# Optimization experiments

Measured on AMD Instinct MI355X. Metric: run time of the kernel, lower is better.

The kernel has to match this reference:

```python
import jax, jax.numpy as jnp
import numpy as np

B, N, D, H = 32, 64, 128, 256

def setup_inputs() -> dict:
    key = jax.random.key(0)
    ks = jax.random.split(key, 6)
    s = 0.02
    return {
        "objects": jax.random.normal(ks[0], (B, N, D), dtype=jnp.float32),
        "gW1": jax.random.normal(ks[1], (2 * D, H), dtype=jnp.float32) * s,
        "gb1": jnp.zeros((H,), dtype=jnp.float32),
        "gW2": jax.random.normal(ks[2], (H, H), dtype=jnp.float32) * s,
        "gb2": jnp.zeros((H,), dtype=jnp.float32),
        "gW3": jax.random.normal(ks[3], (H, H), dtype=jnp.float32) * s,
        "gb3": jnp.zeros((H,), dtype=jnp.float32),
        "fW1": jax.random.normal(ks[4], (H, H), dtype=jnp.float32) * s,
        "fb1": jnp.zeros((H,), dtype=jnp.float32),
        "fW2": jax.random.normal(ks[5], (H, H), dtype=jnp.float32) * s,
        "fb2": jnp.zeros((H,), dtype=jnp.float32),
    }

def reference(objects, gW1, gb1, gW2, gb2, gW3, gb3, fW1, fb1, fW2, fb2):
    b, n, d = objects.shape
    # Pairwise concat: pair[b,i,j] = [objects[b,i], objects[b,j]] -> (B,N,N,2D)
    left = jnp.broadcast_to(objects[:, :, None, :], (b, n, n, d))
    right = jnp.broadcast_to(objects[:, None, :, :], (b, n, n, d))
    pair = jnp.concatenate([left, right], axis=-1)
    # g_theta: 3-layer MLP with ReLU after first two layers
    h = jax.nn.relu(pair @ gW1 + gb1)
    h = jax.nn.relu(h @ gW2 + gb2)
    h = h @ gW3 + gb3                      # (B,N,N,H)
    # Sum over all pairs i != j
    mask = (1.0 - jnp.eye(n, dtype=h.dtype))  # (N,N)
    agg = jnp.einsum('bijh,ij->bh', h, mask)  # (B,H)
    # f_phi: Linear-ReLU-Linear
    out = jax.nn.relu(agg @ fW1 + fb1) @ fW2 + fb2
    return out
```

## Files before the change

### kernel.cpp

```cpp
#include <hip/hip_runtime.h>
#include <hip/hip_bf16.h>

typedef __attribute__((ext_vector_type(8))) _Float16 half8;
typedef __attribute__((ext_vector_type(4))) float f32x4;

union PrepShared {
    struct { float so[8 * 128]; float tt[64 * 65]; } a;
    struct { float sg[8 * 256]; float ps[4][8][256]; } m;
};

__global__ __launch_bounds__(256) void rn_prep(
    const float* __restrict__ obj, const float* __restrict__ gW1,
    const float* __restrict__ gb1, const float* __restrict__ gW2,
    const float* __restrict__ gW3, const float* __restrict__ gb3,
    const float* __restrict__ fW1, const float* __restrict__ fb1,
    _Float16* __restrict__ Lh, _Float16* __restrict__ Rh,
    _Float16* __restrict__ W2h, float* __restrict__ S,
    float* __restrict__ M, float* __restrict__ dvec)
{
    __shared__ PrepShared sh;
    const int blk = blockIdx.x, t = threadIdx.x;

    if (blk < 256) {
        float* so = sh.a.so;
        const int r0 = blk * 8;
        #pragma unroll
        for (int it = 0; it < 4; ++it) so[it * 256 + t] = obj[r0 * 128 + it * 256 + t];
        __syncthreads();
        float accL[8], accR[8];
        #pragma unroll
        for (int r = 0; r < 8; ++r) { accL[r] = 0.f; accR[r] = 0.f; }
        for (int k = 0; k < 128; ++k) {
            float wL = gW1[k * 256 + t];
            float wR = gW1[(128 + k) * 256 + t];
            #pragma unroll
            for (int r = 0; r < 8; ++r) {
                float o = so[r * 128 + k];
                accL[r] += o * wL;
                accR[r] += o * wR;
            }
        }
        float bb = gb1[t];
        #pragma unroll
        for (int r = 0; r < 8; ++r) {
            int row = r0 + r;
            Lh[row * 256 + t] = (_Float16)(accL[r] + bb);
            Rh[row * 256 + t] = (_Float16)accR[r];
        }
    } else if (blk < 272) {
        float* tt = sh.a.tt;
        const int tb = blk - 256;
        const int k0 = (tb >> 2) * 64, c0 = (tb & 3) * 64;
        for (int it = 0; it < 16; ++it) {
            int idx = it * 256 + t, rr = idx >> 6, cc = idx & 63;
            tt[rr * 65 + cc] = gW2[(k0 + rr) * 256 + c0 + cc];
        }
        __syncthreads();
        for (int it = 0; it < 16; ++it) {
            int idx = it * 256 + t, cr = idx >> 6, kk = idx & 63;
            W2h[(c0 + cr) * 256 + (k0 + kk)] = (_Float16)tt[kk * 65 + cr];
        }
    } else if (blk == 272) {
        for (int it = 0; it < 32; ++it) S[it * 256 + t] = 0.f;
        const int cg = t & 63, jq = t >> 6, c0 = cg * 4;
        f32x4 a = (f32x4){0.f, 0.f, 0.f, 0.f};
        #pragma unroll 8
        for (int jj = 0; jj < 64; ++jj) {
            int j = jq * 64 + jj;
            a += gb3[j] * (*(const f32x4*)&fW1[j * 256 + c0]);
        }
        *(f32x4*)&sh.m.ps[jq][0][c0] = a;
        __syncthreads();
        float s = sh.m.ps[0][0][t] + sh.m.ps[1][0][t] + sh.m.ps[2][0][t] + sh.m.ps[3][0][t];
        dvec[t] = 4032.0f * s + fb1[t];
    } else {
        float* sg = sh.m.sg;
        const int r0 = (blk - 273) * 8;
        const int cg = t & 63, jq = t >> 6, c0 = cg * 4;
        #pragma unroll
        for (int it = 0; it < 8; ++it) sg[it * 256 + t] = gW3[(r0 + it) * 256 + t];
        __syncthreads();
        f32x4 acc[8];
        #pragma unroll
        for (int r = 0; r < 8; ++r) acc[r] = (f32x4){0.f, 0.f, 0.f, 0.f};
        #pragma unroll 8
        for (int jj = 0; jj < 64; ++jj) {
            int j = jq * 64 + jj;
            f32x4 wv = *(const f32x4*)&fW1[j * 256 + c0];
            #pragma unroll
            for (int r = 0; r < 8; ++r) acc[r] += sg[r * 256 + j] * wv;
        }
        #pragma unroll
        for (int r = 0; r < 8; ++r) *(f32x4*)&sh.m.ps[jq][r][c0] = acc[r];
        __syncthreads();
        #pragma unroll
        for (int r = 0; r < 8; ++r)
            M[(r0 + r) * 256 + t] =
                sh.m.ps[0][r][t] + sh.m.ps[1][r][t] + sh.m.ps[2][r][t] + sh.m.ps[3][r][t];
    }
}

__global__ __launch_bounds__(512, 1) void rn_main(
    const _Float16* __restrict__ Lh, const _Float16* __restrict__ Rh,
    const _Float16* __restrict__ W2h, const float* __restrict__ gb2,
    float* __restrict__ S)
{
    const int blk = blockIdx.x;
    const int b = blk >> 3, ig = blk & 7;
    const int t = threadIdx.x, lane = t & 63, w = t >> 6;
    const int mg = w >> 2, ng = w & 3;
    const int lc = lane & 15, lg = lane >> 4;

    half8 bfr[4][8];
    #pragma unroll
    for (int n = 0; n < 4; ++n)
        #pragma unroll
        for (int ks = 0; ks < 8; ++ks)
            bfr[n][ks] = *(const half8*)(W2h + (ng * 64 + n * 16 + lc) * 256 + ks * 32 + lg * 8);

    half8 rh[2][8];
    #pragma unroll
    for (int m2 = 0; m2 < 2; ++m2) {
        int row = b * 64 + mg * 32 + m2 * 16 + lc;
        #pragma unroll
        for (int ks = 0; ks < 8; ++ks)
            rh[m2][ks] = *(const half8*)(Rh + row * 256 + ks * 32 + lg * 8);
    }

    float bias[4];
    #pragma unroll
    for (int n = 0; n < 4; ++n) bias[n] = gb2[ng * 64 + n * 16 + lc];

    const _Float16* lbase = Lh + (b * 64 + ig * 8) * 256;
    const half8 zero8 = {(_Float16)0.f, (_Float16)0.f, (_Float16)0.f, (_Float16)0.f,
                         (_Float16)0.f, (_Float16)0.f, (_Float16)0.f, (_Float16)0.f};
    const f32x4 zero4 = (f32x4){0.f, 0.f, 0.f, 0.f};
    float csum[4] = {0.f, 0.f, 0.f, 0.f};

    #pragma unroll 1
    for (int ii = 0; ii < 8; ++ii) {
        f32x4 acc[2][4];
        #pragma unroll
        for (int m2 = 0; m2 < 2; ++m2)
            #pragma unroll
            for (int n = 0; n < 4; ++n)
                acc[m2][n] = zero4;

        #pragma unroll
        for (int ks = 0; ks < 8; ++ks) {
            half8 lhv = *(const half8*)(lbase + ii * 256 + ks * 32 + lg * 8);
            #pragma unroll
            for (int m2 = 0; m2 < 2; ++m2) {
                half8 av = __builtin_elementwise_max(lhv + rh[m2][ks], zero8);
                #pragma unroll
                for (int n = 0; n < 4; ++n)
                    acc[m2][n] = __builtin_amdgcn_mfma_f32_16x16x32_f16(
                        av, bfr[n][ks], acc[m2][n], 0, 0, 0);
            }
        }

        const int iglob = ig * 8 + ii;
        #pragma unroll
        for (int n = 0; n < 4; ++n) {
            #pragma unroll
            for (int m2 = 0; m2 < 2; ++m2) {
                #pragma unroll
                for (int q = 0; q < 4; ++q) {
                    int row = mg * 32 + m2 * 16 + lg * 4 + q;
                    float v = fmaxf(acc[m2][n][q] + bias[n], 0.f);
                    csum[n] += (row == iglob) ? 0.f : v;
                }
            }
        }
    }

    #pragma unroll
    for (int n = 0; n < 4; ++n) {
        float cs = csum[n];
        cs += __shfl_xor(cs, 16);
        cs += __shfl_xor(cs, 32);
        if (lane < 16) atomicAdd(&S[b * 256 + ng * 64 + n * 16 + lc], cs);
    }
}

__global__ __launch_bounds__(1024) void rn_final(
    const float* __restrict__ S, const float* __restrict__ M,
    const float* __restrict__ dvec, const float* __restrict__ fW2,
    const float* __restrict__ fb2, float* __restrict__ out)
{
    __shared__ float vec[256];
    __shared__ float ps[16][260];
    const int b = blockIdx.x, t = threadIdx.x;
    const int cg = t & 63, kq = t >> 6;
    const int c0 = cg * 4;

    if (t < 256) vec[t] = S[b * 256 + t];
    __syncthreads();

    f32x4 w2r[16];
    {
        f32x4 s = (f32x4){0.f, 0.f, 0.f, 0.f};
        #pragma unroll
        for (int kk = 0; kk < 16; ++kk) {
            int k = kq * 16 + kk;
            s += (*(const f32x4*)&M[k * 256 + c0]) * vec[k];
        }
        *(f32x4*)&ps[kq][c0] = s;
        #pragma unroll
        for (int kk = 0; kk < 16; ++kk)
            w2r[kk] = *(const f32x4*)&fW2[(kq * 16 + kk) * 256 + c0];
    }
    __syncthreads();
    if (t < 256) {
        float a = 0.f;
        #pragma unroll
        for (int q = 0; q < 16; ++q) a += ps[q][t];
        vec[t] = fmaxf(a + dvec[t], 0.f);
    }
    __syncthreads();

    {
        f32x4 s = (f32x4){0.f, 0.f, 0.f, 0.f};
        #pragma unroll
        for (int kk = 0; kk < 16; ++kk)
            s += w2r[kk] * vec[kq * 16 + kk];
        *(f32x4*)&ps[kq][c0] = s;
    }
    __syncthreads();
    if (t < 256) {
        float a = 0.f;
        #pragma unroll
        for (int q = 0; q < 16; ++q) a += ps[q][t];
        out[b * 256 + t] = a + fb2[t];
    }
}

extern "C" void kernel_launch(void* const* d_in, const int* in_sizes, int n_in,
                              void* d_out, int out_size, void* d_ws, size_t ws_size,
                              hipStream_t stream)
{
    const float* obj = (const float*)d_in[0];
    const float* gW1 = (const float*)d_in[1];
    const float* gb1 = (const float*)d_in[2];
    const float* gW2 = (const float*)d_in[3];
    const float* gb2 = (const float*)d_in[4];
    const float* gW3 = (const float*)d_in[5];
    const float* gb3 = (const float*)d_in[6];
    const float* fW1 = (const float*)d_in[7];
    const float* fb1 = (const float*)d_in[8];
    const float* fW2 = (const float*)d_in[9];
    const float* fb2 = (const float*)d_in[10];
    float* out = (float*)d_out;

    char* ws = (char*)d_ws;
    _Float16* Lh  = (_Float16*)(ws);
    _Float16* Rh  = (_Float16*)(ws + (1u << 20));
    _Float16* W2h = (_Float16*)(ws + (2u << 20));
    float*    S   = (float*)(ws + (2u << 20) + (128u << 10));
    float*    M   = (float*)(ws + (2u << 20) + (160u << 10));
    float*    dv  = (float*)(ws + (2u << 20) + (416u << 10));

    rn_prep <<<305, 256, 0, stream>>>(obj, gW1, gb1, gW2, gW3, gb3, fW1, fb1,
                                      Lh, Rh, W2h, S, M, dv);
    rn_main <<<256, 512, 0, stream>>>(Lh, Rh, W2h, gb2, S);
    rn_final<<<32, 1024, 0, stream>>>(S, M, dv, fW2, fb2, out);
}
```

Baseline: 52.70 us.

## Stage swizzled R/L tiles in LDS and replace atomics with partial sums

The prep kernel now uses twice as many blocks with 4 rows each, and writes Rh in an XOR-swizzled layout. The main kernel cooperatively loads the batch's R rows and the block's L rows into shared memory and reads them back with the swizzle, avoiding bank conflicts. Per-block column sums are stored to a partial buffer instead of going through atomicAdd, so S no longer has to be zeroed. The final kernel reduces the 16 partials. Launch bounds now allow 2 blocks per CU, which may push the register budget of the main kernel.

```diff
diff --git a/kernel.cpp b/kernel.cpp
--- a/kernel.cpp
+++ b/kernel.cpp
@@ -5,7 +5,7 @@
 typedef __attribute__((ext_vector_type(4))) float f32x4;
 
 union PrepShared {
-    struct { float so[8 * 128]; float tt[64 * 65]; } a;
+    struct { float so[4 * 128]; float tt[64 * 65]; } a;
     struct { float sg[8 * 256]; float ps[4][8][256]; } m;
 };
 
@@ -14,27 +14,26 @@
     const float* __restrict__ gb1, const float* __restrict__ gW2,
     const float* __restrict__ gW3, const float* __restrict__ gb3,
     const float* __restrict__ fW1, const float* __restrict__ fb1,
-    _Float16* __restrict__ Lh, _Float16* __restrict__ Rh,
-    _Float16* __restrict__ W2h, float* __restrict__ S,
-    float* __restrict__ M, float* __restrict__ dvec)
+    _Float16* __restrict__ Lh, char* __restrict__ RhB,
+    _Float16* __restrict__ W2h, float* __restrict__ M, float* __restrict__ dvec)
 {
     __shared__ PrepShared sh;
     const int blk = blockIdx.x, t = threadIdx.x;
 
-    if (blk < 256) {
+    if (blk < 512) {
         float* so = sh.a.so;
-        const int r0 = blk * 8;
-        #pragma unroll
-        for (int it = 0; it < 4; ++it) so[it * 256 + t] = obj[r0 * 128 + it * 256 + t];
-        __syncthreads();
-        float accL[8], accR[8];
-        #pragma unroll
-        for (int r = 0; r < 8; ++r) { accL[r] = 0.f; accR[r] = 0.f; }
+        const int r0 = blk * 4;
+        #pragma unroll
+        for (int it = 0; it < 2; ++it) so[it * 256 + t] = obj[r0 * 128 + it * 256 + t];
+        __syncthreads();
+        float accL[4], accR[4];
+        #pragma unroll
+        for (int r = 0; r < 4; ++r) { accL[r] = 0.f; accR[r] = 0.f; }
         for (int k = 0; k < 128; ++k) {
             float wL = gW1[k * 256 + t];
             float wR = gW1[(128 + k) * 256 + t];
             #pragma unroll
-            for (int r = 0; r < 8; ++r) {
+            for (int r = 0; r < 4; ++r) {
                 float o = so[r * 128 + k];
                 accL[r] += o * wL;
                 accR[r] += o * wR;
@@ -42,14 +41,14 @@
         }
         float bb = gb1[t];
         #pragma unroll
-        for (int r = 0; r < 8; ++r) {
+        for (int r = 0; r < 4; ++r) {
             int row = r0 + r;
             Lh[row * 256 + t] = (_Float16)(accL[r] + bb);
-            Rh[row * 256 + t] = (_Float16)accR[r];
-        }
-    } else if (blk < 272) {
+            *(_Float16*)(RhB + row * 512 + ((2 * t) ^ ((row & 15) << 4))) = (_Float16)accR[r];
+        }
+    } else if (blk < 528) {
         float* tt = sh.a.tt;
-        const int tb = blk - 256;
+        const int tb = blk - 512;
         const int k0 = (tb >> 2) * 64, c0 = (tb & 3) * 64;
         for (int it = 0; it < 16; ++it) {
             int idx = it * 256 + t, rr = idx >> 6, cc = idx & 63;
@@ -60,8 +59,7 @@
             int idx = it * 256 + t, cr = idx >> 6, kk = idx & 63;
             W2h[(c0 + cr) * 256 + (k0 + kk)] = (_Float16)tt[kk * 65 + cr];
         }
-    } else if (blk == 272) {
-        for (int it = 0; it < 32; ++it) S[it * 256 + t] = 0.f;
+    } else if (blk == 528) {
         const int cg = t & 63, jq = t >> 6, c0 = cg * 4;
         f32x4 a = (f32x4){0.f, 0.f, 0.f, 0.f};
         #pragma unroll 8
@@ -75,7 +73,7 @@
         dvec[t] = 4032.0f * s + fb1[t];
     } else {
         float* sg = sh.m.sg;
-        const int r0 = (blk - 273) * 8;
+        const int r0 = (blk - 529) * 8;
         const int cg = t & 63, jq = t >> 6, c0 = cg * 4;
         #pragma unroll
         for (int it = 0; it < 8; ++it) sg[it * 256 + t] = gW3[(r0 + it) * 256 + t];
@@ -100,17 +98,31 @@
     }
 }
 
-__global__ __launch_bounds__(512, 1) void rn_main(
-    const _Float16* __restrict__ Lh, const _Float16* __restrict__ Rh,
+__global__ __launch_bounds__(512, 2) void rn_main(
+    const char* __restrict__ LhB, const char* __restrict__ RhB,
     const _Float16* __restrict__ W2h, const float* __restrict__ gb2,
-    float* __restrict__ S)
-{
+    float* __restrict__ Spart)
+{
+    __shared__ __attribute__((aligned(16))) char smem[36864];
     const int blk = blockIdx.x;
     const int b = blk >> 3, ig = blk & 7;
     const int t = threadIdx.x, lane = t & 63, w = t >> 6;
     const int mg = w >> 2, ng = w & 3;
     const int lc = lane & 15, lg = lane >> 4;
 
+    {
+        const char* gR = RhB + b * 32768;
+        #pragma unroll
+        for (int it = 0; it < 4; ++it) {
+            int u = it * 512 + t;
+            *(f32x4*)(smem + u * 16) = *(const f32x4*)(gR + u * 16);
+        }
+        if (t < 256) {
+            const char* gL = LhB + (b * 64 + ig * 8) * 512;
+            *(f32x4*)(smem + 32768 + t * 16) = *(const f32x4*)(gL + t * 16);
+        }
+    }
+
     half8 bfr[4][8];
     #pragma unroll
     for (int n = 0; n < 4; ++n)
@@ -118,37 +130,38 @@
         for (int ks = 0; ks < 8; ++ks)
             bfr[n][ks] = *(const half8*)(W2h + (ng * 64 + n * 16 + lc) * 256 + ks * 32 + lg * 8);
 
+    float bias[4];
+    #pragma unroll
+    for (int n = 0; n < 4; ++n) bias[n] = gb2[ng * 64 + n * 16 + lc];
+
+    __syncthreads();
+
     half8 rh[2][8];
     #pragma unroll
     for (int m2 = 0; m2 < 2; ++m2) {
-        int row = b * 64 + mg * 32 + m2 * 16 + lc;
-        #pragma unroll
-        for (int ks = 0; ks < 8; ++ks)
-            rh[m2][ks] = *(const half8*)(Rh + row * 256 + ks * 32 + lg * 8);
-    }
-
-    float bias[4];
-    #pragma unroll
-    for (int n = 0; n < 4; ++n) bias[n] = gb2[ng * 64 + n * 16 + lc];
-
-    const _Float16* lbase = Lh + (b * 64 + ig * 8) * 256;
+        int row = mg * 32 + m2 * 16 + lc;
+        #pragma unroll
+        for (int ks = 0; ks < 8; ++ks) {
+            int kb = ks * 64 + lg * 16;
+            rh[m2][ks] = *(const half8*)(smem + row * 512 + (kb ^ (lc << 4)));
+        }
+    }
+
     const half8 zero8 = {(_Float16)0.f, (_Float16)0.f, (_Float16)0.f, (_Float16)0.f,
                          (_Float16)0.f, (_Float16)0.f, (_Float16)0.f, (_Float16)0.f};
-    const f32x4 zero4 = (f32x4){0.f, 0.f, 0.f, 0.f};
     float csum[4] = {0.f, 0.f, 0.f, 0.f};
 
-    #pragma unroll 1
     for (int ii = 0; ii < 8; ++ii) {
         f32x4 acc[2][4];
         #pragma unroll
         for (int m2 = 0; m2 < 2; ++m2)
             #pragma unroll
             for (int n = 0; n < 4; ++n)
-                acc[m2][n] = zero4;
+                acc[m2][n] = (f32x4){0.f, 0.f, 0.f, 0.f};
 
         #pragma unroll
         for (int ks = 0; ks < 8; ++ks) {
-            half8 lhv = *(const half8*)(lbase + ii * 256 + ks * 32 + lg * 8);
+            half8 lhv = *(const half8*)(smem + 32768 + ii * 512 + ks * 64 + lg * 16);
             #pragma unroll
             for (int m2 = 0; m2 < 2; ++m2) {
                 half8 av = __builtin_elementwise_max(lhv + rh[m2][ks], zero8);
@@ -162,15 +175,16 @@
         const int iglob = ig * 8 + ii;
         #pragma unroll
         for (int n = 0; n < 4; ++n) {
-            #pragma unroll
-            for (int m2 = 0; m2 < 2; ++m2) {
+            float cs = 0.f;
+            #pragma unroll
+            for (int m2 = 0; m2 < 2; ++m2)
                 #pragma unroll
                 for (int q = 0; q < 4; ++q) {
                     int row = mg * 32 + m2 * 16 + lg * 4 + q;
                     float v = fmaxf(acc[m2][n][q] + bias[n], 0.f);
-                    csum[n] += (row == iglob) ? 0.f : v;
+                    cs += (row == iglob) ? 0.f : v;
                 }
-            }
+            csum[n] += cs;
         }
     }
 
@@ -179,12 +193,13 @@
         float cs = csum[n];
         cs += __shfl_xor(cs, 16);
         cs += __shfl_xor(cs, 32);
-        if (lane < 16) atomicAdd(&S[b * 256 + ng * 64 + n * 16 + lc], cs);
+        if (lane < 16)
+            Spart[((b * 8 + ig) * 2 + mg) * 256 + ng * 64 + n * 16 + lc] = cs;
     }
 }
 
 __global__ __launch_bounds__(1024) void rn_final(
-    const float* __restrict__ S, const float* __restrict__ M,
+    const float* __restrict__ Spart, const float* __restrict__ M,
     const float* __restrict__ dvec, const float* __restrict__ fW2,
     const float* __restrict__ fb2, float* __restrict__ out)
 {
@@ -194,7 +209,12 @@
     const int cg = t & 63, kq = t >> 6;
     const int c0 = cg * 4;
 
-    if (t < 256) vec[t] = S[b * 256 + t];
+    if (t < 256) {
+        float a = 0.f;
+        #pragma unroll
+        for (int p = 0; p < 16; ++p) a += Spart[(b * 16 + p) * 256 + t];
+        vec[t] = a;
+    }
     __syncthreads();
 
     f32x4 w2r[16];
@@ -253,15 +273,15 @@
     float* out = (float*)d_out;
 
     char* ws = (char*)d_ws;
-    _Float16* Lh  = (_Float16*)(ws);
-    _Float16* Rh  = (_Float16*)(ws + (1u << 20));
-    _Float16* W2h = (_Float16*)(ws + (2u << 20));
-    float*    S   = (float*)(ws + (2u << 20) + (128u << 10));
-    float*    M   = (float*)(ws + (2u << 20) + (160u << 10));
-    float*    dv  = (float*)(ws + (2u << 20) + (416u << 10));
-
-    rn_prep <<<305, 256, 0, stream>>>(obj, gW1, gb1, gW2, gW3, gb3, fW1, fb1,
-                                      Lh, Rh, W2h, S, M, dv);
-    rn_main <<<256, 512, 0, stream>>>(Lh, Rh, W2h, gb2, S);
-    rn_final<<<32, 1024, 0, stream>>>(S, M, dv, fW2, fb2, out);
-}
+    _Float16* Lh    = (_Float16*)(ws);
+    char*     RhB   = ws + (1u << 20);
+    _Float16* W2h   = (_Float16*)(ws + (2u << 20));
+    float*    Spart = (float*)(ws + (2u << 20) + (128u << 10));
+    float*    M     = (float*)(ws + (2u << 20) + (640u << 10));
+    float*    dv    = (float*)(ws + (2u << 20) + (896u << 10));
+
+    rn_prep <<<561, 256, 0, stream>>>(obj, gW1, gb1, gW2, gW3, gb3, fW1, fb1,
+                                      Lh, RhB, W2h, M, dv);
+    rn_main <<<256, 512, 0, stream>>>((const char*)Lh, RhB, W2h, gb2, Spart);
+    rn_final<<<32, 1024, 0, stream>>>(Spart, M, dv, fW2, fb2, out);
+}
```

Measured after the change: 50.43 us. -4.3%, faster.
